# Optimization experiments

Hardware: AMD Instinct MI355X
Metric: run time of the kernel (lower is better)

The kernel has to match this reference:

```python
import jax, jax.numpy as jnp
import numpy as np

N_NODES = 10000
N_EDGES = 640000
D_FEAT = 128


def setup_inputs() -> dict:
    key = jax.random.key(0)
    k1, k2, k3 = jax.random.split(key, 3)
    feat = jax.random.normal(k1, (N_NODES, D_FEAT), dtype=jnp.float32)
    src = jax.random.randint(k2, (N_EDGES,), 0, N_NODES, dtype=jnp.int64)
    dst = jax.random.randint(k3, (N_EDGES,), 0, N_NODES, dtype=jnp.int64)
    return {"feat": feat, "src": src, "dst": dst}


def reference(feat, src, dst):
    # GraphConv with weight=False, in_feats == out_feats, norm='both'.
    # Executed path (else-branch of the source): sum-aggregate messages
    # copy_u/sum, then scale by in_degree^{-0.5}. (The out-degree norm is
    # dead code on this path in the given source.)
    n = feat.shape[0]
    # SpMM: gather source features along edges, scatter-add into destinations
    h = jax.ops.segment_sum(feat[src], dst, num_segments=n)  # [N, D]
    deg_in = jax.ops.segment_sum(jnp.ones(dst.shape, feat.dtype), dst, num_segments=n)
    norm = jnp.maximum(deg_in, 1.0) ** -0.5  # clamp(min=1) then pow(-0.5)
    return h * norm[:, None]
```

## Files before the change

### kernel.cpp

```cpp
#include <hip/hip_runtime.h>

#define D_FEAT 128
#define NPP 16
#define QCAP 128
#define PCAP 12
#define MAX_NPART 640
#define OVF_PB 32
#define LOCAL_OVF 64
#define BIN_THREADS 512
#define EPB (BIN_THREADS * 4)

typedef unsigned int u32;

__device__ __forceinline__ u32 f2bf(float f) {
    u32 x = __float_as_uint(f);
    return (x + 0x7FFFu + ((x >> 16) & 1u)) >> 16;
}
__device__ __forceinline__ float bf_lo(u32 u) { return __uint_as_float(u << 16); }
__device__ __forceinline__ float bf_hi(u32 u) { return __uint_as_float(u & 0xFFFF0000u); }

__global__ __launch_bounds__(BIN_THREADS) void bin_kernel(
        const int* __restrict__ src, const int* __restrict__ dst,
        const float* __restrict__ feat, u32* __restrict__ fbf,
        int* __restrict__ povf_cnt, int* __restrict__ povf,
        u32* __restrict__ bins,
        int n_edges, int npart, int nblk, int npacks) {
    __shared__ u32 stage[MAX_NPART * PCAP];
    __shared__ int lcnt[MAX_NPART];
    __shared__ int bovf_cnt;
    int tid = threadIdx.x;
    int b = blockIdx.x;

    for (int i = b * BIN_THREADS + tid; i < npacks;
         i += gridDim.x * BIN_THREADS) {
        float4 v = ((const float4*)feat)[i];
        u32 a = f2bf(v.x) | (f2bf(v.y) << 16);
        u32 c = f2bf(v.z) | (f2bf(v.w) << 16);
        ((uint2*)fbf)[i] = make_uint2(a, c);
    }

    for (int i = tid; i < npart; i += BIN_THREADS) lcnt[i] = 0;
    if (tid == 0) bovf_cnt = 0;
    __syncthreads();

    int base = b * EPB + tid * 4;
    int s0 = 0, s1 = 0, s2 = 0, s3 = 0, d0 = -1, d1 = -1, d2 = -1, d3 = -1;
    if (base + 3 < n_edges) {
        int4 sv = ((const int4*)src)[base >> 2];
        int4 dv = ((const int4*)dst)[base >> 2];
        s0 = sv.x; s1 = sv.y; s2 = sv.z; s3 = sv.w;
        d0 = dv.x; d1 = dv.y; d2 = dv.z; d3 = dv.w;
    } else if (base < n_edges) {
        if (base + 0 < n_edges) { s0 = src[base + 0]; d0 = dst[base + 0]; }
        if (base + 1 < n_edges) { s1 = src[base + 1]; d1 = dst[base + 1]; }
        if (base + 2 < n_edges) { s2 = src[base + 2]; d2 = dst[base + 2]; }
    }
    #define RANK(dK, sK)                                                      \
        if (dK >= 0) {                                                        \
            int pK = dK >> 4;                                                 \
            int r = atomicAdd(&lcnt[pK], 1);                                  \
            if (r < PCAP) {                                                   \
                stage[pK * PCAP + r] = ((u32)(dK & 15) << 14) | (u32)sK;      \
            } else {                                                          \
                int o = atomicAdd(&bovf_cnt, 1);                              \
                if (o < OVF_PB)                                               \
                    povf[b * OVF_PB + o] = ((dK) << 14) | (sK);               \
            }                                                                 \
        }
    RANK(d0, s0)
    RANK(d1, s1)
    RANK(d2, s2)
    RANK(d3, s3)
    #undef RANK
    __syncthreads();

    for (int p2 = tid; p2 < npart; p2 += BIN_THREADS) {
        int c = lcnt[p2]; if (c > PCAP) c = PCAP;
        stage[p2 * PCAP] = (stage[p2 * PCAP] & 0x3FFFFu) | ((u32)c << 24);
    }
    __syncthreads();

    uint4* dd4 = (uint4*)(bins + (size_t)b * npart * PCAP);
    const uint4* ss4 = (const uint4*)stage;
    int nv = npart * PCAP / 4;
    for (int i = tid; i < nv; i += BIN_THREADS) dd4[i] = ss4[i];
    if (tid == 0) {
        int c = bovf_cnt; if (c > OVF_PB) c = OVF_PB;
        povf_cnt[b] = c;
    }
}

__global__ __launch_bounds__(256) void gather_kernel(
        const u32* __restrict__ fbf, const u32* __restrict__ bins,
        const int* __restrict__ povf_cnt, const int* __restrict__ povf,
        float* __restrict__ out, int n_nodes, int npart, int nblk) {
    __shared__ __attribute__((aligned(16))) int sq[NPP * QCAP];
    __shared__ int scnt[NPP];
    __shared__ int sdeg[NPP];
    __shared__ int sovf[LOCAL_OVF];
    __shared__ int lovf[LOCAL_OVF];
    __shared__ int sovf_cnt, lovf_cnt;
    int tid = threadIdx.x;
    int p = blockIdx.x;
    int bstart = p * NPP;
    if (tid < NPP) { scnt[tid] = 0; sdeg[tid] = 0; }
    if (tid == 0) { sovf_cnt = 0; lovf_cnt = 0; }
    __syncthreads();

    #define PUSHE(eV) {                                                       \
        u32 e_ = (eV);                                                        \
        int s_ = (int)(e_ & 0x3FFFu);                                         \
        int dl_ = (int)((e_ >> 14) & 0xFu);                                   \
        int pos_ = atomicAdd(&scnt[dl_], 1);                                  \
        if (pos_ < QCAP) sq[dl_ * QCAP + pos_] = s_;                          \
        else { int o_ = atomicAdd(&lovf_cnt, 1);                              \
               if (o_ < LOCAL_OVF) lovf[o_] = (int)(e_ & 0x3FFFFu); } }

    for (int q2 = tid; q2 < nblk; q2 += 256) {
        const uint4* cell4 = (const uint4*)(bins + ((size_t)q2 * npart + p) * PCAP);
        uint4 A = cell4[0];
        int c = (int)(A.x >> 24);
        if (c > 0) {
            PUSHE(A.x); if (c > 1) PUSHE(A.y);
            if (c > 2) PUSHE(A.z); if (c > 3) PUSHE(A.w);
            if (c > 4) {
                uint4 B = cell4[1];
                PUSHE(B.x); if (c > 5) PUSHE(B.y);
                if (c > 6) PUSHE(B.z); if (c > 7) PUSHE(B.w);
                if (c > 8) {
                    uint4 C = cell4[2];
                    PUSHE(C.x); if (c > 9) PUSHE(C.y);
                    if (c > 10) PUSHE(C.z); if (c > 11) PUSHE(C.w);
                }
            }
        }
        int oc = povf_cnt[q2];
        if (oc < 0) oc = 0; if (oc > OVF_PB) oc = OVF_PB;
        for (int r = 0; r < oc; ++r) {
            int ent = povf[q2 * OVF_PB + r];
            int d = (ent >> 14) & 0x3FFF;
            if ((d >> 4) == p) {
                atomicAdd(&sdeg[d & 15], 1);
                int o = atomicAdd(&sovf_cnt, 1);
                if (o < LOCAL_OVF) sovf[o] = ent;
            }
        }
    }
    #undef PUSHE
    __syncthreads();

    int g  = tid >> 4;
    int gl = tid & 15;
    const uint4* f4 = (const uint4*)fbf;
    int node = bstart + g;
    if (node < n_nodes) {
        int full = scnt[g] + sdeg[g];
        int degq = scnt[g] < QCAP ? scnt[g] : QCAP;
        const int* qq = &sq[g * QCAP];
        float a0 = 0.f, a1 = 0.f, a2 = 0.f, a3 = 0.f;
        float a4 = 0.f, a5 = 0.f, a6 = 0.f, a7 = 0.f;
        int i = 0;
        for (; i + 4 <= degq; i += 4) {
            int4 s4 = *(const int4*)&qq[i];
            uint4 u0 = f4[(size_t)s4.x * 16 + gl];
            uint4 u1 = f4[(size_t)s4.y * 16 + gl];
            uint4 u2 = f4[(size_t)s4.z * 16 + gl];
            uint4 u3 = f4[(size_t)s4.w * 16 + gl];
            a0 += bf_lo(u0.x); a1 += bf_hi(u0.x); a2 += bf_lo(u0.y); a3 += bf_hi(u0.y);
            a4 += bf_lo(u0.z); a5 += bf_hi(u0.z); a6 += bf_lo(u0.w); a7 += bf_hi(u0.w);
            a0 += bf_lo(u1.x); a1 += bf_hi(u1.x); a2 += bf_lo(u1.y); a3 += bf_hi(u1.y);
            a4 += bf_lo(u1.z); a5 += bf_hi(u1.z); a6 += bf_lo(u1.w); a7 += bf_hi(u1.w);
            a0 += bf_lo(u2.x); a1 += bf_hi(u2.x); a2 += bf_lo(u2.y); a3 += bf_hi(u2.y);
            a4 += bf_lo(u2.z); a5 += bf_hi(u2.z); a6 += bf_lo(u2.w); a7 += bf_hi(u2.w);
            a0 += bf_lo(u3.x); a1 += bf_hi(u3.x); a2 += bf_lo(u3.y); a3 += bf_hi(u3.y);
            a4 += bf_lo(u3.z); a5 += bf_hi(u3.z); a6 += bf_lo(u3.w); a7 += bf_hi(u3.w);
        }
        for (; i < degq; ++i) {
            uint4 u = f4[(size_t)qq[i] * 16 + gl];
            a0 += bf_lo(u.x); a1 += bf_hi(u.x); a2 += bf_lo(u.y); a3 += bf_hi(u.y);
            a4 += bf_lo(u.z); a5 += bf_hi(u.z); a6 += bf_lo(u.w); a7 += bf_hi(u.w);
        }
        float sc = rsqrtf((float)(full > 1 ? full : 1));
        float4 r0 = { a0 * sc, a1 * sc, a2 * sc, a3 * sc };
        float4 r1 = { a4 * sc, a5 * sc, a6 * sc, a7 * sc };
        ((float4*)out)[(size_t)node * 32 + gl * 2 + 0] = r0;
        ((float4*)out)[(size_t)node * 32 + gl * 2 + 1] = r1;
    }
    __syncthreads();

    int lc = lovf_cnt; if (lc > LOCAL_OVF) lc = LOCAL_OVF;
    for (int k = g; k < lc; k += NPP) {
        int ent = lovf[k];
        int dl = (ent >> 14) & 15;
        int s = ent & 0x3FFF;
        int full = scnt[dl] + sdeg[dl];
        float sc = rsqrtf((float)(full > 1 ? full : 1));
        uint4 u = f4[(size_t)s * 16 + gl];
        float* orow = out + (size_t)(bstart + dl) * D_FEAT + gl * 8;
        atomicAdd(&orow[0], bf_lo(u.x) * sc);
        atomicAdd(&orow[1], bf_hi(u.x) * sc);
        atomicAdd(&orow[2], bf_lo(u.y) * sc);
        atomicAdd(&orow[3], bf_hi(u.y) * sc);
        atomicAdd(&orow[4], bf_lo(u.z) * sc);
        atomicAdd(&orow[5], bf_hi(u.z) * sc);
        atomicAdd(&orow[6], bf_lo(u.w) * sc);
        atomicAdd(&orow[7], bf_hi(u.w) * sc);
    }
    int oc2 = sovf_cnt; if (oc2 > LOCAL_OVF) oc2 = LOCAL_OVF;
    for (int k = g; k < oc2; k += NPP) {
        int ent = sovf[k];
        int dl = (ent >> 14) & 15;
        int s = ent & 0x3FFF;
        int full = scnt[dl] + sdeg[dl];
        float sc = rsqrtf((float)(full > 1 ? full : 1));
        uint4 u = f4[(size_t)s * 16 + gl];
        float* orow = out + (size_t)(bstart + dl) * D_FEAT + gl * 8;
        atomicAdd(&orow[0], bf_lo(u.x) * sc);
        atomicAdd(&orow[1], bf_hi(u.x) * sc);
        atomicAdd(&orow[2], bf_lo(u.y) * sc);
        atomicAdd(&orow[3], bf_hi(u.y) * sc);
        atomicAdd(&orow[4], bf_lo(u.z) * sc);
        atomicAdd(&orow[5], bf_hi(u.z) * sc);
        atomicAdd(&orow[6], bf_lo(u.w) * sc);
        atomicAdd(&orow[7], bf_hi(u.w) * sc);
    }
}


__global__ void zero_kernel(float* __restrict__ out, float* __restrict__ deg,
                            int n_out, int n_deg) {
    int i = blockIdx.x * blockDim.x + threadIdx.x;
    if (i < n_out) out[i] = 0.0f;
    if (i < n_deg) deg[i] = 0.0f;
}

__global__ void scatter_kernel(const float* __restrict__ feat,
                               const int* __restrict__ src,
                               const int* __restrict__ dst,
                               float* __restrict__ out,
                               float* __restrict__ deg,
                               int n_edges) {
    long long gid = (long long)blockIdx.x * blockDim.x + threadIdx.x;
    int e = (int)(gid >> 7);
    int f = (int)(gid & 127);
    if (e >= n_edges) return;
    int s = src[e];
    int d = dst[e];
    float v = feat[(long long)s * D_FEAT + f];
    atomicAdd(&out[(long long)d * D_FEAT + f], v);
    if (f == 0) atomicAdd(&deg[d], 1.0f);
}

__global__ void norm_kernel(float* __restrict__ out, const float* __restrict__ deg,
                            int n_out) {
    int gid = blockIdx.x * blockDim.x + threadIdx.x;
    if (gid >= n_out) return;
    int i = gid >> 7;
    float dg = fmaxf(deg[i], 1.0f);
    out[gid] = out[gid] * rsqrtf(dg);
}

extern "C" void kernel_launch(void* const* d_in, const int* in_sizes, int n_in,
                              void* d_out, int out_size, void* d_ws, size_t ws_size,
                              hipStream_t stream) {
    const float* feat = (const float*)d_in[0];
    const int*   src  = (const int*)d_in[1];
    const int*   dst  = (const int*)d_in[2];
    float* out = (float*)d_out;

    const int n_edges = in_sizes[1];
    const int n_out   = out_size;
    const int n_nodes = n_out / D_FEAT;

    int npart  = (n_nodes + NPP - 1) / NPP;
    int nblk   = (n_edges + EPB - 1) / EPB;
    int npacks = n_out / 4;

    size_t head = ((size_t)nblk + (size_t)nblk * OVF_PB + 3) & ~(size_t)3;
    size_t bins_ints = (size_t)nblk * npart * PCAP;
    size_t fbf_off = (head + bins_ints + 3) & ~(size_t)3;
    size_t need = (fbf_off + (size_t)n_out / 2) * sizeof(int);

    if (ws_size >= need && npart <= MAX_NPART && n_nodes <= 16384) {
        int* povf_cnt = (int*)d_ws;
        int* povf     = povf_cnt + nblk;
        u32* bins     = (u32*)d_ws + head;
        u32* fbf      = (u32*)d_ws + fbf_off;

        bin_kernel<<<nblk, BIN_THREADS, 0, stream>>>(
            src, dst, feat, fbf, povf_cnt, povf, bins,
            n_edges, npart, nblk, npacks);
        gather_kernel<<<npart, 256, 0, stream>>>(
            fbf, bins, povf_cnt, povf, out, n_nodes, npart, nblk);
    } else {
        float* deg = (float*)d_ws;
        {
            int threads = 256;
            int blocks = (n_out + threads - 1) / threads;
            zero_kernel<<<blocks, threads, 0, stream>>>(out, deg, n_out, n_nodes);
        }
        {
            long long total = (long long)n_edges * D_FEAT;
            int threads = 256;
            int blocks = (int)((total + threads - 1) / threads);
            scatter_kernel<<<blocks, threads, 0, stream>>>(feat, src, dst, out, deg, n_edges);
        }
        {
            int threads = 256;
            int blocks = (n_out + threads - 1) / threads;
            norm_kernel<<<blocks, threads, 0, stream>>>(out, deg, n_out);
        }
    }
}
```

Measured before the change: 32.25 us.

## Double bin block size, widen partition cells, pad stage stride, unroll gather by 8

The binning kernel now runs 1024 threads per block with 16-entry partition cells (up from 12) and a padded shared stage stride of 17. The copy-out to global memory changes from uint4 to scalar writes. The gather loop is unrolled to eight outstanding feature loads per iteration to increase memory-level parallelism. Fewer binning blocks means fewer cells for the gather to scan, but larger cells mean more global bin traffic and slower scalar copy-out.

```diff
diff --git a/kernel.cpp b/kernel.cpp
--- a/kernel.cpp
+++ b/kernel.cpp
@@ -3,11 +3,12 @@
 #define D_FEAT 128
 #define NPP 16
 #define QCAP 128
-#define PCAP 12
+#define PCAP 16
+#define SSTRIDE 17
 #define MAX_NPART 640
-#define OVF_PB 32
+#define OVF_PB 64
 #define LOCAL_OVF 64
-#define BIN_THREADS 512
+#define BIN_THREADS 1024
 #define EPB (BIN_THREADS * 4)
 
 typedef unsigned int u32;
@@ -25,7 +26,7 @@
         int* __restrict__ povf_cnt, int* __restrict__ povf,
         u32* __restrict__ bins,
         int n_edges, int npart, int nblk, int npacks) {
-    __shared__ u32 stage[MAX_NPART * PCAP];
+    __shared__ u32 stage[MAX_NPART * SSTRIDE];
     __shared__ int lcnt[MAX_NPART];
     __shared__ int bovf_cnt;
     int tid = threadIdx.x;
@@ -60,7 +61,7 @@
             int pK = dK >> 4;                                                 \
             int r = atomicAdd(&lcnt[pK], 1);                                  \
             if (r < PCAP) {                                                   \
-                stage[pK * PCAP + r] = ((u32)(dK & 15) << 14) | (u32)sK;      \
+                stage[pK * SSTRIDE + r] = ((u32)(dK & 15) << 14) | (u32)sK;   \
             } else {                                                          \
                 int o = atomicAdd(&bovf_cnt, 1);                              \
                 if (o < OVF_PB)                                               \
@@ -76,14 +77,15 @@
 
     for (int p2 = tid; p2 < npart; p2 += BIN_THREADS) {
         int c = lcnt[p2]; if (c > PCAP) c = PCAP;
-        stage[p2 * PCAP] = (stage[p2 * PCAP] & 0x3FFFFu) | ((u32)c << 24);
-    }
-    __syncthreads();
-
-    uint4* dd4 = (uint4*)(bins + (size_t)b * npart * PCAP);
-    const uint4* ss4 = (const uint4*)stage;
-    int nv = npart * PCAP / 4;
-    for (int i = tid; i < nv; i += BIN_THREADS) dd4[i] = ss4[i];
+        stage[p2 * SSTRIDE] = (stage[p2 * SSTRIDE] & 0x3FFFFu) |
+                              ((u32)c << 24);
+    }
+    __syncthreads();
+
+    u32* bout = bins + (size_t)b * npart * PCAP;
+    int nw = npart * PCAP;
+    for (int i = tid; i < nw; i += BIN_THREADS)
+        bout[i] = stage[(i >> 4) * SSTRIDE + (i & 15)];
     if (tid == 0) {
         int c = bovf_cnt; if (c > OVF_PB) c = OVF_PB;
         povf_cnt[b] = c;
@@ -131,6 +133,11 @@
                     uint4 C = cell4[2];
                     PUSHE(C.x); if (c > 9) PUSHE(C.y);
                     if (c > 10) PUSHE(C.z); if (c > 11) PUSHE(C.w);
+                    if (c > 12) {
+                        uint4 D = cell4[3];
+                        PUSHE(D.x); if (c > 13) PUSHE(D.y);
+                        if (c > 14) PUSHE(D.z); if (c > 15) PUSHE(D.w);
+                    }
                 }
             }
         }
@@ -160,26 +167,36 @@
         float a0 = 0.f, a1 = 0.f, a2 = 0.f, a3 = 0.f;
         float a4 = 0.f, a5 = 0.f, a6 = 0.f, a7 = 0.f;
         int i = 0;
+        #define ACC(U)                                                        \
+            a0 += bf_lo(U.x); a1 += bf_hi(U.x); a2 += bf_lo(U.y);             \
+            a3 += bf_hi(U.y); a4 += bf_lo(U.z); a5 += bf_hi(U.z);             \
+            a6 += bf_lo(U.w); a7 += bf_hi(U.w);
+        for (; i + 8 <= degq; i += 8) {
+            int4 sA = *(const int4*)&qq[i];
+            int4 sB = *(const int4*)&qq[i + 4];
+            uint4 u0 = f4[(size_t)sA.x * 16 + gl];
+            uint4 u1 = f4[(size_t)sA.y * 16 + gl];
+            uint4 u2 = f4[(size_t)sA.z * 16 + gl];
+            uint4 u3 = f4[(size_t)sA.w * 16 + gl];
+            uint4 u4 = f4[(size_t)sB.x * 16 + gl];
+            uint4 u5 = f4[(size_t)sB.y * 16 + gl];
+            uint4 u6 = f4[(size_t)sB.z * 16 + gl];
+            uint4 u7 = f4[(size_t)sB.w * 16 + gl];
+            ACC(u0) ACC(u1) ACC(u2) ACC(u3) ACC(u4) ACC(u5) ACC(u6) ACC(u7)
+        }
         for (; i + 4 <= degq; i += 4) {
-            int4 s4 = *(const int4*)&qq[i];
-            uint4 u0 = f4[(size_t)s4.x * 16 + gl];
-            uint4 u1 = f4[(size_t)s4.y * 16 + gl];
-            uint4 u2 = f4[(size_t)s4.z * 16 + gl];
-            uint4 u3 = f4[(size_t)s4.w * 16 + gl];
-            a0 += bf_lo(u0.x); a1 += bf_hi(u0.x); a2 += bf_lo(u0.y); a3 += bf_hi(u0.y);
-            a4 += bf_lo(u0.z); a5 += bf_hi(u0.z); a6 += bf_lo(u0.w); a7 += bf_hi(u0.w);
-            a0 += bf_lo(u1.x); a1 += bf_hi(u1.x); a2 += bf_lo(u1.y); a3 += bf_hi(u1.y);
-            a4 += bf_lo(u1.z); a5 += bf_hi(u1.z); a6 += bf_lo(u1.w); a7 += bf_hi(u1.w);
-            a0 += bf_lo(u2.x); a1 += bf_hi(u2.x); a2 += bf_lo(u2.y); a3 += bf_hi(u2.y);
-            a4 += bf_lo(u2.z); a5 += bf_hi(u2.z); a6 += bf_lo(u2.w); a7 += bf_hi(u2.w);
-            a0 += bf_lo(u3.x); a1 += bf_hi(u3.x); a2 += bf_lo(u3.y); a3 += bf_hi(u3.y);
-            a4 += bf_lo(u3.z); a5 += bf_hi(u3.z); a6 += bf_lo(u3.w); a7 += bf_hi(u3.w);
+            int4 sA = *(const int4*)&qq[i];
+            uint4 u0 = f4[(size_t)sA.x * 16 + gl];
+            uint4 u1 = f4[(size_t)sA.y * 16 + gl];
+            uint4 u2 = f4[(size_t)sA.z * 16 + gl];
+            uint4 u3 = f4[(size_t)sA.w * 16 + gl];
+            ACC(u0) ACC(u1) ACC(u2) ACC(u3)
         }
         for (; i < degq; ++i) {
             uint4 u = f4[(size_t)qq[i] * 16 + gl];
-            a0 += bf_lo(u.x); a1 += bf_hi(u.x); a2 += bf_lo(u.y); a3 += bf_hi(u.y);
-            a4 += bf_lo(u.z); a5 += bf_hi(u.z); a6 += bf_lo(u.w); a7 += bf_hi(u.w);
-        }
+            ACC(u)
+        }
+        #undef ACC
         float sc = rsqrtf((float)(full > 1 ? full : 1));
         float4 r0 = { a0 * sc, a1 * sc, a2 * sc, a3 * sc };
         float4 r1 = { a4 * sc, a5 * sc, a6 * sc, a7 * sc };
```

After: 31.83 us. Within noise of the previous version (-1.3%).
